# Kernel tuning notes

Hardware: AMD Instinct MI355X
Metric: run time of the kernel (lower is better)

## Reference

```python
import jax, jax.numpy as jnp
import numpy as np

B, T, C, H = 4, 2048, 768, 12
D = C // H  # head dim = 64


def setup_inputs() -> dict:
    key = jax.random.key(0)
    ks = jax.random.split(key, 4)
    scale = 0.02
    return {
        "x": jax.random.normal(ks[0], (B, T, C), dtype=jnp.float32),
        "W_attn": jax.random.normal(ks[1], (C, 3 * C), dtype=jnp.float32) * scale,
        "b_attn": jnp.zeros((3 * C,), dtype=jnp.float32),
        "W_proj": jax.random.normal(ks[2], (C, C), dtype=jnp.float32) * scale,
        "b_proj": jnp.zeros((C,), dtype=jnp.float32),
    }


def reference(x, W_attn, b_attn, W_proj, b_proj):
    Bsz, Tlen, Cdim = x.shape
    qkv = x @ W_attn + b_attn                    # [B,T,3C]
    q, k, v = jnp.split(qkv, 3, axis=-1)          # each [B,T,C]
    # [B,T,C] -> [B,H,T,D]
    def heads(t):
        return t.reshape(Bsz, Tlen, H, D).transpose(0, 2, 1, 3)
    q, k, v = heads(q), heads(k), heads(v)
    att = jnp.einsum("bhqd,bhkd->bhqk", q, k) * (1.0 / np.sqrt(D))
    # causal mask: position q attends to k <= q
    mask = jnp.tril(jnp.ones((Tlen, Tlen), dtype=bool))
    att = jnp.where(mask[None, None], att, -jnp.inf)
    att = jax.nn.softmax(att, axis=-1)
    y = jnp.einsum("bhqk,bhkd->bhqd", att, v)     # [B,H,T,D]
    y = y.transpose(0, 2, 1, 3).reshape(Bsz, Tlen, Cdim)
    return y @ W_proj + b_proj
```

## Files before the change

kernel.cpp:

```cpp
#include <hip/hip_runtime.h>

#define B_SZ   4
#define T_LEN  2048
#define C_DIM  768
#define H_NUM  12
#define THREEC (3 * C_DIM)

typedef _Float16 f16;
typedef _Float16 half8 __attribute__((ext_vector_type(8)));
typedef _Float16 half4 __attribute__((ext_vector_type(4)));
typedef float    f32x4 __attribute__((ext_vector_type(4)));

#define GLD16(gaddr, laddr)                                                         \
  __builtin_amdgcn_global_load_lds(                                                 \
      (const __attribute__((address_space(1))) unsigned int*)(gaddr),               \
      (__attribute__((address_space(3))) unsigned int*)(laddr), 16, 0, 0)
#define MFMA16(a, b, c) __builtin_amdgcn_mfma_f32_16x16x32_f16(a, b, c, 0, 0, 0)

__global__ __launch_bounds__(256) void cast_f32_f16_kernel(
    const float* __restrict__ src, f16* __restrict__ dst, int n8) {
  int i = blockIdx.x * 256 + threadIdx.x;
  if (i >= n8) return;
  const float* s = src + (size_t)i * 8;
  half8 h;
#pragma unroll
  for (int u = 0; u < 8; ++u) h[u] = (f16)s[u];
  *(half8*)(dst + (size_t)i * 8) = h;
}

__global__ __launch_bounds__(256) void transpose_cast2_kernel(
    const float* __restrict__ Wa, const float* __restrict__ Wp,
    f16* __restrict__ WtA, f16* __restrict__ WtP) {
  __shared__ f16 tile[32][33];
  int bx = blockIdx.x;
  const float* W; f16* Wt; int N;
  if (bx < THREEC / 32) { W = Wa; Wt = WtA; N = THREEC; }
  else { W = Wp; Wt = WtP; N = C_DIM; bx -= THREEC / 32; }
  const int n0 = bx * 32, k0 = blockIdx.y * 32;
  const int tx = threadIdx.x & 31, ty = threadIdx.x >> 5;
#pragma unroll
  for (int i = 0; i < 4; ++i)
    tile[ty + i * 8][tx] = (f16)W[(size_t)(k0 + ty + i * 8) * N + n0 + tx];
  __syncthreads();
#pragma unroll
  for (int i = 0; i < 4; ++i)
    Wt[(size_t)(n0 + ty + i * 8) * C_DIM + k0 + tx] = tile[tx][ty + i * 8];
}

template <int BM, int BN, int OUT_F16>
__global__ __launch_bounds__(256) void gemm_f16_kernel(
    const f16* __restrict__ A, const f16* __restrict__ Bt,
    const float* __restrict__ bias, f16* __restrict__ OutH,
    float* __restrict__ OutF, int M, int N, int K) {
  __shared__ f16 As[BM * 64];
  __shared__ f16 Bs[BN * 64];
  const int tid = threadIdx.x;
  const int lane = tid & 63, wave = tid >> 6;
  const int lm = lane & 15, kq = lane >> 4, lm7 = lm & 7;
  constexpr int MT = BM / 32, NT = BN / 32;
  const int wm = (wave & 1) * (BM / 2), wn = (wave >> 1) * (BN / 2);
  const int row0 = blockIdx.y * BM, col0 = blockIdx.x * BN;

  f32x4 acc[MT][NT] = {};

  for (int k0 = 0; k0 < K; k0 += 64) {
    __syncthreads();
#pragma unroll
    for (int i = 0; i < BM / 32; ++i) {
      int c = tid + i * 256;
      int r = c >> 3, cc = (c & 7) ^ (r & 7);
      GLD16(&A[(size_t)(row0 + r) * K + k0 + cc * 8],
            &As[(i * 256 + wave * 64) * 8]);
    }
#pragma unroll
    for (int i = 0; i < BN / 32; ++i) {
      int c = tid + i * 256;
      int r = c >> 3, cc = (c & 7) ^ (r & 7);
      GLD16(&Bt[(size_t)(col0 + r) * K + k0 + cc * 8],
            &Bs[(i * 256 + wave * 64) * 8]);
    }
    __syncthreads();
#pragma unroll
    for (int ks = 0; ks < 2; ++ks) {
      const int pos = (ks * 4 + kq);
      half8 af[MT], bf[NT];
#pragma unroll
      for (int t = 0; t < MT; ++t)
        af[t] = *(const half8*)&As[(wm + t * 16 + lm) * 64 + (pos ^ lm7) * 8];
#pragma unroll
      for (int t = 0; t < NT; ++t)
        bf[t] = *(const half8*)&Bs[(wn + t * 16 + lm) * 64 + (pos ^ lm7) * 8];
#pragma unroll
      for (int mt = 0; mt < MT; ++mt)
#pragma unroll
        for (int nt = 0; nt < NT; ++nt)
          acc[mt][nt] = MFMA16(af[mt], bf[nt], acc[mt][nt]);
    }
  }

#pragma unroll
  for (int mt = 0; mt < MT; ++mt) {
    const int row = row0 + wm + mt * 16 + kq * 4;
#pragma unroll
    for (int nt = 0; nt < NT; ++nt) {
      const int col = col0 + wn + nt * 16 + lm;
      const float bv = bias[col];
#pragma unroll
      for (int r = 0; r < 4; ++r) {
        float v = acc[mt][nt][r] + bv;
        if (OUT_F16)
          OutH[(size_t)(row + r) * N + col] = (f16)v;
        else
          OutF[(size_t)(row + r) * N + col] = v;
      }
    }
  }
}

__global__ __launch_bounds__(256) void v_transpose_kernel(
    const f16* __restrict__ qkv, f16* __restrict__ vt) {
  __shared__ f16 tile[64 * 68];
  const int bh = blockIdx.x, b = bh / H_NUM, h = bh % H_NUM;
  const int t0 = blockIdx.y * 64;
  const int tid = threadIdx.x;
#pragma unroll
  for (int i = 0; i < 2; ++i) {
    int c = tid + i * 256;
    int tr = c >> 3, doff = (c & 7) * 8;
    half8 v = *(const half8*)&qkv[(size_t)(b * T_LEN + t0 + tr) * THREEC + 2 * C_DIM + h * 64 + doff];
#pragma unroll
    for (int u = 0; u < 8; ++u) tile[(doff + u) * 68 + tr] = v[u];
  }
  __syncthreads();
#pragma unroll
  for (int i = 0; i < 2; ++i) {
    int c = tid + i * 256;
    int d = c >> 3, toff = (c & 7) * 8;
    half8 v;
#pragma unroll
    for (int u = 0; u < 8; ++u) v[u] = tile[d * 68 + toff + u];
    *(half8*)&vt[((size_t)bh * 64 + d) * T_LEN + t0 + toff] = v;
  }
}

__global__ __launch_bounds__(256) void attn_kernel(
    const f16* __restrict__ qkv, const f16* __restrict__ vt,
    f16* __restrict__ y) {
  __shared__ f16 Kt[64 * 64];
  __shared__ f16 Vt[64 * 64];
  __shared__ f16 Pl[4][16 * 64];

  const int bh = blockIdx.x, b = bh / H_NUM, h = bh % H_NUM;
  const int tid = threadIdx.x, lane = tid & 63, wave = tid >> 6;
  const int lm = lane & 15, kq = lane >> 4, lm7 = lm & 7;
  const f16 qscale = (f16)(0.125f * 1.44269504f);

  half8 vones;
#pragma unroll
  for (int u = 0; u < 8; ++u) vones[u] = (f16)1.f;

  int srow[2], scol[2];
#pragma unroll
  for (int i = 0; i < 2; ++i) {
    int s = tid + i * 256;
    srow[i] = s >> 3;
    scol[i] = ((s & 7) ^ (srow[i] & 7)) * 8;
  }

  for (int hf = 0; hf < 2; ++hf) {
    const int c = (hf == 0) ? (31 - (int)blockIdx.y) : (int)blockIdx.y;
    const int q0 = c * 64;
    const int qw = q0 + wave * 16;

    half8 bq[2];
#pragma unroll
    for (int c2 = 0; c2 < 2; ++c2) {
      half8 v = *(const half8*)&qkv[(size_t)(b * T_LEN + qw + lm) * THREEC +
                                    h * 64 + c2 * 32 + kq * 8];
      bq[c2] = v * qscale;
    }

    f32x4 o[4] = {};
    f32x4 ol = {};

    const f16* kp[2];
    const f16* vp[2];
#pragma unroll
    for (int i = 0; i < 2; ++i) {
      kp[i] = &qkv[(size_t)(b * T_LEN + srow[i]) * THREEC + C_DIM + h * 64 + scol[i]];
      vp[i] = &vt[((size_t)bh * 64 + srow[i]) * T_LEN + scol[i]];
    }

    const int n_tiles = c + 1;
    for (int it = 0; it < n_tiles; ++it) {
      const int j0 = it * 64;
      __syncthreads();
#pragma unroll
      for (int i = 0; i < 2; ++i) {
        GLD16(kp[i], &Kt[(i * 256 + wave * 64) * 8]);
        kp[i] += (size_t)64 * THREEC;
        GLD16(vp[i], &Vt[(i * 256 + wave * 64) * 8]);
        vp[i] += 64;
      }
      __syncthreads();

      f32x4 s4[4];
#pragma unroll
      for (int ct = 0; ct < 4; ++ct) {
        const f16* kr = &Kt[(ct * 16 + lm) * 64];
        half8 ak0 = *(const half8*)&kr[(kq ^ lm7) * 8];
        half8 ak1 = *(const half8*)&kr[((4 + kq) ^ lm7) * 8];
        f32x4 z = {};
        z = MFMA16(ak0, bq[0], z);
        s4[ct] = MFMA16(ak1, bq[1], z);
      }
      if (it == n_tiles - 1) {
        const int qrow = qw + lm;
#pragma unroll
        for (int ct = 0; ct < 4; ++ct)
#pragma unroll
          for (int r = 0; r < 4; ++r)
            if (j0 + ct * 16 + kq * 4 + r > qrow) s4[ct][r] = -1e30f;
      }
      f16* prow = &Pl[wave][lm * 64];
#pragma unroll
      for (int ct = 0; ct < 4; ++ct) {
        half4 pk;
#pragma unroll
        for (int r = 0; r < 4; ++r) pk[r] = (f16)exp2f(s4[ct][r]);
        *(half4*)&prow[(((ct * 2 + (kq >> 1)) ^ lm7) * 8) + (kq & 1) * 4] = pk;
      }
      __asm__ volatile("s_waitcnt lgkmcnt(0)" ::: "memory");
      half8 ap0 = *(const half8*)&prow[(kq ^ lm7) * 8];
      half8 ap1 = *(const half8*)&prow[((4 + kq) ^ lm7) * 8];
#pragma unroll
      for (int dt = 0; dt < 4; ++dt) {
        const f16* vr = &Vt[(dt * 16 + lm) * 64];
        half8 bv0 = *(const half8*)&vr[(kq ^ lm7) * 8];
        half8 bv1 = *(const half8*)&vr[((4 + kq) ^ lm7) * 8];
        o[dt] = MFMA16(ap0, bv0, o[dt]);
        o[dt] = MFMA16(ap1, bv1, o[dt]);
      }
      ol = MFMA16(ap0, vones, ol);
      ol = MFMA16(ap1, vones, ol);
    }

#pragma unroll
    for (int r = 0; r < 4; ++r) {
      const float inv = 1.f / ol[r];
      const size_t base =
          (size_t)(b * T_LEN + qw + kq * 4 + r) * C_DIM + h * 64;
#pragma unroll
      for (int dt = 0; dt < 4; ++dt)
        y[base + dt * 16 + lm] = (f16)(o[dt][r] * inv);
    }
  }
}

extern "C" void kernel_launch(void* const* d_in, const int* in_sizes, int n_in,
                              void* d_out, int out_size, void* d_ws, size_t ws_size,
                              hipStream_t stream) {
  const float* x      = (const float*)d_in[0];
  const float* W_attn = (const float*)d_in[1];
  const float* b_attn = (const float*)d_in[2];
  const float* W_proj = (const float*)d_in[3];
  const float* b_proj = (const float*)d_in[4];
  float* out = (float*)d_out;

  const int M = B_SZ * T_LEN;
  auto align256 = [](size_t v) { return (v + 255) & ~(size_t)255; };
  char* ws = (char*)d_ws;
  f16* xh   = (f16*)ws; ws += align256((size_t)M * C_DIM * 2);
  f16* WtA  = (f16*)ws; ws += align256((size_t)THREEC * C_DIM * 2);
  f16* WtP  = (f16*)ws; ws += align256((size_t)C_DIM * C_DIM * 2);
  f16* qkvh = (f16*)ws; ws += align256((size_t)M * THREEC * 2);
  f16* vtg  = (f16*)ws; ws += align256((size_t)B_SZ * H_NUM * 64 * T_LEN * 2);
  f16* yh   = (f16*)ws; ws += align256((size_t)M * C_DIM * 2);

  {
    int n8 = M * C_DIM / 8;
    cast_f32_f16_kernel<<<(n8 + 255) / 256, 256, 0, stream>>>(x, xh, n8);
  }
  transpose_cast2_kernel<<<dim3((THREEC + C_DIM) / 32, C_DIM / 32), 256, 0, stream>>>(
      W_attn, W_proj, WtA, WtP);

  gemm_f16_kernel<128, 128, 1><<<dim3(THREEC / 128, M / 128), 256, 0, stream>>>(
      xh, WtA, b_attn, qkvh, nullptr, M, THREEC, C_DIM);

  v_transpose_kernel<<<dim3(B_SZ * H_NUM, T_LEN / 64), 256, 0, stream>>>(qkvh, vtg);

  attn_kernel<<<dim3(B_SZ * H_NUM, 16), 256, 0, stream>>>(qkvh, vtg, yh);

  gemm_f16_kernel<128, 64, 0><<<dim3(C_DIM / 64, M / 128), 256, 0, stream>>>(
      yh, WtP, b_proj, nullptr, out, M, C_DIM, C_DIM);
}
```

Baseline: 210.2 us.

## Process paired causal query chunks concurrently in one 512-thread block sharing K/V tiles

Before, each block handled two query chunks (a late one and an early one) one after the other, loading K/V tiles separately for each. Now the block has 8 waves: four handle the late chunk and four the early chunk, and both read the same K/V tile from shared memory. The shared prefix of K/V is therefore loaded once, and there are more waves per block to hide latency. In exchange, the early-chunk waves sit idle during the tail tiles, and the larger block with launch bounds (512,6) may limit registers and occupancy.

```diff
diff --git a/kernel.cpp b/kernel.cpp
--- a/kernel.cpp
+++ b/kernel.cpp
@@ -143,67 +143,53 @@
   }
 }
 
-__global__ __launch_bounds__(256) void attn_kernel(
+__global__ __launch_bounds__(512, 6) void attn_kernel(
     const f16* __restrict__ qkv, const f16* __restrict__ vt,
     f16* __restrict__ y) {
   __shared__ f16 Kt[64 * 64];
   __shared__ f16 Vt[64 * 64];
-  __shared__ f16 Pl[4][16 * 64];
+  __shared__ f16 Pl[8][16 * 64];
 
   const int bh = blockIdx.x, b = bh / H_NUM, h = bh % H_NUM;
+  const int yb = blockIdx.y;
   const int tid = threadIdx.x, lane = tid & 63, wave = tid >> 6;
   const int lm = lane & 15, kq = lane >> 4, lm7 = lm & 7;
+  const int cw = (wave < 4) ? (31 - yb) : yb;
+  const int qw = cw * 64 + (wave & 3) * 16;
   const f16 qscale = (f16)(0.125f * 1.44269504f);
 
   half8 vones;
 #pragma unroll
   for (int u = 0; u < 8; ++u) vones[u] = (f16)1.f;
 
-  int srow[2], scol[2];
-#pragma unroll
-  for (int i = 0; i < 2; ++i) {
-    int s = tid + i * 256;
-    srow[i] = s >> 3;
-    scol[i] = ((s & 7) ^ (srow[i] & 7)) * 8;
-  }
-
-  for (int hf = 0; hf < 2; ++hf) {
-    const int c = (hf == 0) ? (31 - (int)blockIdx.y) : (int)blockIdx.y;
-    const int q0 = c * 64;
-    const int qw = q0 + wave * 16;
-
-    half8 bq[2];
-#pragma unroll
-    for (int c2 = 0; c2 < 2; ++c2) {
-      half8 v = *(const half8*)&qkv[(size_t)(b * T_LEN + qw + lm) * THREEC +
-                                    h * 64 + c2 * 32 + kq * 8];
-      bq[c2] = v * qscale;
-    }
-
-    f32x4 o[4] = {};
-    f32x4 ol = {};
-
-    const f16* kp[2];
-    const f16* vp[2];
-#pragma unroll
-    for (int i = 0; i < 2; ++i) {
-      kp[i] = &qkv[(size_t)(b * T_LEN + srow[i]) * THREEC + C_DIM + h * 64 + scol[i]];
-      vp[i] = &vt[((size_t)bh * 64 + srow[i]) * T_LEN + scol[i]];
-    }
-
-    const int n_tiles = c + 1;
-    for (int it = 0; it < n_tiles; ++it) {
-      const int j0 = it * 64;
-      __syncthreads();
-#pragma unroll
-      for (int i = 0; i < 2; ++i) {
-        GLD16(kp[i], &Kt[(i * 256 + wave * 64) * 8]);
-        kp[i] += (size_t)64 * THREEC;
-        GLD16(vp[i], &Vt[(i * 256 + wave * 64) * 8]);
-        vp[i] += 64;
-      }
-      __syncthreads();
-
+  half8 bq[2];
+#pragma unroll
+  for (int c2 = 0; c2 < 2; ++c2) {
+    half8 v = *(const half8*)&qkv[(size_t)(b * T_LEN + qw + lm) * THREEC +
+                                  h * 64 + c2 * 32 + kq * 8];
+    bq[c2] = v * qscale;
+  }
+
+  f32x4 o[4] = {};
+  f32x4 ol = {};
+
+  const int srow = tid >> 3;
+  const int scol = ((tid & 7) ^ (srow & 7)) * 8;
+  const f16* kp = &qkv[(size_t)(b * T_LEN + srow) * THREEC + C_DIM + h * 64 + scol];
+  const f16* vp = &vt[((size_t)bh * 64 + srow) * T_LEN + scol];
+
+  f16* prow = &Pl[wave][lm * 64];
+
+  const int n_tiles = 32 - yb;
+  for (int it = 0; it < n_tiles; ++it) {
+    __syncthreads();
+    GLD16(kp, &Kt[(wave * 64) * 8]);
+    kp += (size_t)64 * THREEC;
+    GLD16(vp, &Vt[(wave * 64) * 8]);
+    vp += 64;
+    __syncthreads();
+
+    if (it <= cw) {
       f32x4 s4[4];
 #pragma unroll
       for (int ct = 0; ct < 4; ++ct) {
@@ -214,15 +200,14 @@
         z = MFMA16(ak0, bq[0], z);
         s4[ct] = MFMA16(ak1, bq[1], z);
       }
-      if (it == n_tiles - 1) {
-        const int qrow = qw + lm;
+      if (it == cw) {
+        const int qrow = qw + lm, j0 = it * 64;
 #pragma unroll
         for (int ct = 0; ct < 4; ++ct)
 #pragma unroll
           for (int r = 0; r < 4; ++r)
             if (j0 + ct * 16 + kq * 4 + r > qrow) s4[ct][r] = -1e30f;
       }
-      f16* prow = &Pl[wave][lm * 64];
 #pragma unroll
       for (int ct = 0; ct < 4; ++ct) {
         half4 pk;
@@ -244,16 +229,16 @@
       ol = MFMA16(ap0, vones, ol);
       ol = MFMA16(ap1, vones, ol);
     }
-
-#pragma unroll
-    for (int r = 0; r < 4; ++r) {
-      const float inv = 1.f / ol[r];
-      const size_t base =
-          (size_t)(b * T_LEN + qw + kq * 4 + r) * C_DIM + h * 64;
-#pragma unroll
-      for (int dt = 0; dt < 4; ++dt)
-        y[base + dt * 16 + lm] = (f16)(o[dt][r] * inv);
-    }
+  }
+
+#pragma unroll
+  for (int r = 0; r < 4; ++r) {
+    const float inv = 1.f / ol[r];
+    const size_t base =
+        (size_t)(b * T_LEN + qw + kq * 4 + r) * C_DIM + h * 64;
+#pragma unroll
+    for (int dt = 0; dt < 4; ++dt)
+      y[base + dt * 16 + lm] = (f16)(o[dt][r] * inv);
   }
 }
 
@@ -289,7 +274,7 @@
 
   v_transpose_kernel<<<dim3(B_SZ * H_NUM, T_LEN / 64), 256, 0, stream>>>(qkvh, vtg);
 
-  attn_kernel<<<dim3(B_SZ * H_NUM, 16), 256, 0, stream>>>(qkvh, vtg, yh);
+  attn_kernel<<<dim3(B_SZ * H_NUM, 16), 512, 0, stream>>>(qkvh, vtg, yh);
 
   gemm_f16_kernel<128, 64, 0><<<dim3(C_DIM / 64, M / 128), 256, 0, stream>>>(
       yh, WtP, b_proj, nullptr, out, M, C_DIM, C_DIM);
```

Measured after the change: 204.0 us. -2.9%, faster.
